# Performance work log

Hardware: AMD Instinct MI355X
Metric: run time of the kernel (lower is better)

The kernel has to match this reference:

```python
import jax, jax.numpy as jnp
import numpy as np

E = 512
H = 8
D = E // H  # 64
B = 2
S = 4096


def setup_inputs() -> dict:
    key = jax.random.key(0)
    ks = jax.random.split(key, 12)
    s = 1.0 / np.sqrt(E)
    return {
        "x": jax.random.normal(ks[0], (B, S, E), dtype=jnp.float32),
        "bias": jax.random.normal(ks[1], (H, 1, S, S), dtype=jnp.float32),
        "mask": jax.random.randint(ks[2], (1, 1, S, S), 0, 2, dtype=jnp.int32),
        "Wq": jax.random.normal(ks[3], (E, E), dtype=jnp.float32) * s,
        "bq": jnp.zeros((E,), dtype=jnp.float32),
        "Wk": jax.random.normal(ks[4], (E, E), dtype=jnp.float32) * s,
        "bk": jnp.zeros((E,), dtype=jnp.float32),
        "Wv": jax.random.normal(ks[5], (E, E), dtype=jnp.float32) * s,
        "bv": jnp.zeros((E,), dtype=jnp.float32),
        "Wo": jax.random.normal(ks[6], (E, E), dtype=jnp.float32) * s,
        "bo": jnp.zeros((E,), dtype=jnp.float32),
    }


def _split_heads(t):
    # [B,S,E] -> [H,B,S,D]  (matches x.view(B,-1,H,D).permute(2,0,1,3))
    b, s, _ = t.shape
    return t.reshape(b, s, H, D).transpose(2, 0, 1, 3)


def reference(x, bias, mask, Wq, bq, Wk, bk, Wv, bv, Wo, bo):
    # torch Linear: y = x @ W.T + b
    q = _split_heads(x @ Wq.T + bq)  # [H,B,S,D]
    k = _split_heads(x @ Wk.T + bk)
    v = _split_heads(x @ Wv.T + bv)

    scores = jnp.einsum("hbqd,hbkd->hbqk", q, k) + bias  # [H,B,S,S]
    scores = jnp.where(mask == 0, jnp.float32(-1e20), scores)
    # NOTE: original divides AFTER bias-add and masking
    probs = jax.nn.softmax(scores / jnp.sqrt(jnp.float32(D)), axis=-1)
    out = jnp.einsum("hbqk,hbkd->hbqd", probs, v)  # [H,B,S,D]
    out = out.transpose(1, 2, 0, 3).reshape(x.shape[0], -1, H * D)  # [B,S,E]
    return out @ Wo.T + bo
```

## Files before the change

### kernel.cpp

```cpp
#include <hip/hip_runtime.h>
#include <hip/hip_bf16.h>

typedef __bf16 bf16x8 __attribute__((ext_vector_type(8)));
typedef float f32x4 __attribute__((ext_vector_type(4)));

#define S_LEN 4096
#define EMB   512
#define NHEAD 8
#define HDIM  64
#define NBAT  2
#define NROW  (NBAT * S_LEN)

static __device__ __forceinline__ f32x4 mfma16x16(bf16x8 a, bf16x8 b, f32x4 c) {
    return __builtin_amdgcn_mfma_f32_16x16x32_bf16(a, b, c, 0, 0, 0);
}

__global__ __launch_bounds__(256) void convert_kernel(
    const float* __restrict__ x, const float* __restrict__ Wq,
    const float* __restrict__ Wk, const float* __restrict__ Wv,
    const float* __restrict__ Wo,
    __hip_bfloat16* __restrict__ xb, __hip_bfloat16* __restrict__ wqkv,
    __hip_bfloat16* __restrict__ wob)
{
    const int NX = NROW * EMB;
    const int NW = EMB * EMB;
    int i = blockIdx.x * 256 + threadIdx.x;
    if (i < NX) { xb[i] = __float2bfloat16(x[i]); return; }
    int j = i - NX;
    if (j < 3 * NW) {
        int p = j >> 18, r = j & (NW - 1);
        const float* src = (p == 0) ? Wq : (p == 1) ? Wk : Wv;
        wqkv[j] = __float2bfloat16(src[r]);
    } else if (j < 4 * NW) {
        int r = j - 3 * NW;
        wob[r] = __float2bfloat16(Wo[r]);
    }
}

__device__ __forceinline__ void gemm_core(
    const __hip_bfloat16* __restrict__ A, const __hip_bfloat16* __restrict__ Bw,
    int mbase, int nbase,
    __hip_bfloat16* As, __hip_bfloat16* Bs, f32x4 acc[2][4])
{
    const int tid = threadIdx.x;
    const int w = tid >> 6, lane = tid & 63, l = lane & 15, quad = lane >> 4;
    const f32x4 zero = {0.f, 0.f, 0.f, 0.f};
#pragma unroll
    for (int mb = 0; mb < 2; mb++)
#pragma unroll
        for (int nb = 0; nb < 4; nb++) acc[mb][nb] = zero;

    const int r0 = tid >> 2, kc = tid & 3;
    const __hip_bfloat16* pa0 = A + (size_t)(mbase + r0) * EMB + kc * 8;
    const __hip_bfloat16* pa1 = pa0 + (size_t)64 * EMB;
    const __hip_bfloat16* pb  = Bw + (size_t)(nbase + r0) * EMB + kc * 8;

    uint4 va0 = *(const uint4*)pa0;
    uint4 va1 = *(const uint4*)pa1;
    uint4 vb  = *(const uint4*)pb;

    for (int k0 = 0; k0 < EMB; k0 += 32) {
        __syncthreads();
        *(uint4*)(As + r0 * 40 + kc * 8)        = va0;
        *(uint4*)(As + (r0 + 64) * 40 + kc * 8) = va1;
        *(uint4*)(Bs + r0 * 40 + kc * 8)        = vb;
        __syncthreads();
        if (k0 + 32 < EMB) {
            va0 = *(const uint4*)(pa0 + k0 + 32);
            va1 = *(const uint4*)(pa1 + k0 + 32);
            vb  = *(const uint4*)(pb  + k0 + 32);
        }
        bf16x8 af[2], bfr[4];
#pragma unroll
        for (int mb = 0; mb < 2; mb++)
            af[mb] = *(const bf16x8*)(As + (w * 32 + mb * 16 + l) * 40 + quad * 8);
#pragma unroll
        for (int nb = 0; nb < 4; nb++)
            bfr[nb] = *(const bf16x8*)(Bs + (nb * 16 + l) * 40 + quad * 8);
        __builtin_amdgcn_s_setprio(1);
#pragma unroll
        for (int mb = 0; mb < 2; mb++)
#pragma unroll
            for (int nb = 0; nb < 4; nb++)
                acc[mb][nb] = mfma16x16(af[mb], bfr[nb], acc[mb][nb]);
        __builtin_amdgcn_s_setprio(0);
    }
}

__global__ __launch_bounds__(256, 4) void qkv_gemm(
    const __hip_bfloat16* __restrict__ xb, const __hip_bfloat16* __restrict__ wqkv,
    const float* __restrict__ bq, const float* __restrict__ bk, const float* __restrict__ bv,
    __hip_bfloat16* __restrict__ Qh, __hip_bfloat16* __restrict__ Kh,
    __hip_bfloat16* __restrict__ Vt)
{
    __shared__ __align__(16) __hip_bfloat16 As[128 * 40];
    __shared__ __align__(16) __hip_bfloat16 Bs[64 * 40];
    const int mbase = blockIdx.x * 128, nbase = blockIdx.y * 64;
    f32x4 acc[2][4];
    gemm_core(xb, wqkv, mbase, nbase, As, Bs, acc);

    const int tid = threadIdx.x;
    const int w = tid >> 6, lane = tid & 63, l = lane & 15, quad = lane >> 4;
    const int p = nbase >> 9;
    const float* bias = (p == 0) ? bq : (p == 1) ? bk : bv;
    __hip_bfloat16* dst = (p == 0) ? Qh : (p == 1) ? Kh : Vt;
#pragma unroll
    for (int mb = 0; mb < 2; mb++)
#pragma unroll
        for (int nb = 0; nb < 4; nb++)
#pragma unroll
            for (int r = 0; r < 4; r++) {
                int m = mbase + w * 32 + mb * 16 + quad * 4 + r;
                int n = nbase + nb * 16 + l;
                int o = n & 511;
                float v = acc[mb][nb][r] + bias[o];
                int b = m >> 12, s = m & 4095, hh = o >> 6, d = o & 63;
                size_t idx = (p == 2)
                    ? ((size_t)((hh * 2 + b) * 64 + d)) * 4096 + s
                    : ((size_t)((hh * 2 + b) * 4096 + s)) * 64 + d;
                dst[idx] = __float2bfloat16(v);
            }
}

__global__ __launch_bounds__(256, 2) void attn_kernel(
    const __hip_bfloat16* __restrict__ Qh, const __hip_bfloat16* __restrict__ Kh,
    const __hip_bfloat16* __restrict__ Vt,
    const float* __restrict__ bias, const int* __restrict__ mask,
    __hip_bfloat16* __restrict__ Om)
{
    const int h = blockIdx.x, qt = blockIdx.y;
    const int tid = threadIdx.x;
    const int w = tid >> 6, lane = tid & 63, l = lane & 15, quad = lane >> 4;
    const int q0 = qt * 64;
    const float CS = 0.18033688011112042f;

    __shared__ __align__(16) __hip_bfloat16 Ks[2][64 * 72];
    __shared__ __align__(16) __hip_bfloat16 Vs[2][64 * 72];
    __shared__ __align__(16) __hip_bfloat16 Ps[64 * 72];
    __shared__ __align__(16) float Bor[64 * 68];

    bf16x8 qf[2][2];
#pragma unroll
    for (int b = 0; b < 2; b++) {
        const __hip_bfloat16* qp =
            Qh + ((size_t)((h * 2 + b) * 4096 + q0 + w * 16 + l)) * 64;
        qf[b][0] = *(const bf16x8*)(qp + quad * 8);
        qf[b][1] = *(const bf16x8*)(qp + 32 + quad * 8);
    }

    f32x4 oacc[2][4];
    float mst[2][4], lst[2][4];
    const f32x4 zero = {0.f, 0.f, 0.f, 0.f};
#pragma unroll
    for (int b = 0; b < 2; b++) {
#pragma unroll
        for (int nb = 0; nb < 4; nb++) oacc[b][nb] = zero;
#pragma unroll
        for (int r = 0; r < 4; r++) { mst[b][r] = -__builtin_inff(); lst[b][r] = 0.f; }
    }

    const int krow = tid >> 3, kch = tid & 7;
    const int ldso0 = krow * 72 + kch * 8;
    const int ldso1 = ldso0 + 32 * 72;
    int koff[8];
#pragma unroll
    for (int j = 0; j < 8; j++) {
        int b = (j >> 1) & 1, isV = j >> 2;
        int row = (j & 1) * 32 + krow;
        koff[j] = isV
            ? ((h * 2 + b) * 64 + row) * 4096 + kch * 8
            : ((h * 2 + b) * 4096 + row) * 64 + kch * 8;
    }
    const float* biasH = bias + (size_t)h * S_LEN * S_LEN;
    int bmo[4], bro[4];
#pragma unroll
    for (int j = 0; j < 4; j++) {
        int d = j * 256 + tid, row = d >> 4, c4 = d & 15;
        bmo[j] = (q0 + row) * S_LEN + c4 * 4;
        bro[j] = row * 68 + c4 * 4;
    }

    uint4  kv[8];
    float4 bv4[4];
    int4   mv4[4];
#pragma unroll
    for (int j = 0; j < 8; j++)
        kv[j] = (j >> 2) ? *(const uint4*)(Vt + koff[j])
                         : *(const uint4*)(Kh + koff[j]);
#pragma unroll
    for (int j = 0; j < 4; j++) {
        bv4[j] = *(const float4*)(biasH + bmo[j]);
        mv4[j] = *(const int4*)(mask + bmo[j]);
    }

    for (int kt = 0; kt < 64; kt++) {
        __syncthreads();
#pragma unroll
        for (int j = 0; j < 8; j++) {
            int lo = (j & 1) ? ldso1 : ldso0;
            if (j >> 2) *(uint4*)(Vs[(j >> 1) & 1] + lo) = kv[j];
            else        *(uint4*)(Ks[(j >> 1) & 1] + lo) = kv[j];
        }
#pragma unroll
        for (int j = 0; j < 4; j++) {
            float4 t;
            t.x = mv4[j].x ? bv4[j].x * CS : -1e30f;
            t.y = mv4[j].y ? bv4[j].y * CS : -1e30f;
            t.z = mv4[j].z ? bv4[j].z * CS : -1e30f;
            t.w = mv4[j].w ? bv4[j].w * CS : -1e30f;
            *(float4*)(Bor + bro[j]) = t;
        }
        __syncthreads();

        if (kt < 63) {
            const int k0 = (kt + 1) * 64;
#pragma unroll
            for (int j = 0; j < 8; j++)
                kv[j] = (j >> 2) ? *(const uint4*)(Vt + koff[j] + k0)
                                 : *(const uint4*)(Kh + koff[j] + k0 * 64);
#pragma unroll
            for (int j = 0; j < 4; j++) {
                bv4[j] = *(const float4*)(biasH + bmo[j] + k0);
                mv4[j] = *(const int4*)(mask + bmo[j] + k0);
            }
        }

        float borr[4][4];
#pragma unroll
        for (int nb = 0; nb < 4; nb++)
#pragma unroll
            for (int r = 0; r < 4; r++)
                borr[nb][r] = Bor[(w * 16 + quad * 4 + r) * 68 + nb * 16 + l];

#pragma unroll
        for (int b = 0; b < 2; b++) {
            f32x4 sc[4] = {zero, zero, zero, zero};
            __builtin_amdgcn_s_setprio(1);
#pragma unroll
            for (int ks = 0; ks < 2; ks++)
#pragma unroll
                for (int nb = 0; nb < 4; nb++) {
                    bf16x8 kf = *(const bf16x8*)(Ks[b] + (nb * 16 + l) * 72 + ks * 32 + quad * 8);
                    sc[nb] = mfma16x16(qf[b][ks], kf, sc[nb]);
                }
            __builtin_amdgcn_s_setprio(0);
            float xv[4][4], rmax[4];
#pragma unroll
            for (int r = 0; r < 4; r++) rmax[r] = -__builtin_inff();
#pragma unroll
            for (int nb = 0; nb < 4; nb++)
#pragma unroll
                for (int r = 0; r < 4; r++) {
                    xv[nb][r] = fmaf(sc[nb][r], CS, borr[nb][r]);
                    rmax[r] = fmaxf(rmax[r], xv[nb][r]);
                }
#pragma unroll
            for (int r = 0; r < 4; r++) {
                rmax[r] = fmaxf(rmax[r], __shfl_xor(rmax[r], 1));
                rmax[r] = fmaxf(rmax[r], __shfl_xor(rmax[r], 2));
                rmax[r] = fmaxf(rmax[r], __shfl_xor(rmax[r], 4));
                rmax[r] = fmaxf(rmax[r], __shfl_xor(rmax[r], 8));
            }
            float alpha[4], rsum[4];
#pragma unroll
            for (int r = 0; r < 4; r++) {
                float mn = fmaxf(mst[b][r], rmax[r]);
                alpha[r] = __builtin_amdgcn_exp2f(mst[b][r] - mn);
                mst[b][r] = mn;
                rsum[r] = 0.f;
            }
#pragma unroll
            for (int nb = 0; nb < 4; nb++)
#pragma unroll
                for (int r = 0; r < 4; r++) {
                    float e = __builtin_amdgcn_exp2f(xv[nb][r] - mst[b][r]);
                    rsum[r] += e;
                    Ps[(w * 16 + quad * 4 + r) * 72 + nb * 16 + l] =
                        __float2bfloat16(e);
                }
#pragma unroll
            for (int r = 0; r < 4; r++) {
                rsum[r] += __shfl_xor(rsum[r], 1);
                rsum[r] += __shfl_xor(rsum[r], 2);
                rsum[r] += __shfl_xor(rsum[r], 4);
                rsum[r] += __shfl_xor(rsum[r], 8);
                lst[b][r] = lst[b][r] * alpha[r] + rsum[r];
            }
#pragma unroll
            for (int nb = 0; nb < 4; nb++)
#pragma unroll
                for (int r = 0; r < 4; r++) oacc[b][nb][r] *= alpha[r];
            __builtin_amdgcn_s_setprio(1);
#pragma unroll
            for (int ks = 0; ks < 2; ks++) {
                bf16x8 pf = *(const bf16x8*)(Ps + (w * 16 + l) * 72 + ks * 32 + quad * 8);
#pragma unroll
                for (int nb = 0; nb < 4; nb++) {
                    bf16x8 vf = *(const bf16x8*)(Vs[b] + (nb * 16 + l) * 72 + ks * 32 + quad * 8);
                    oacc[b][nb] = mfma16x16(pf, vf, oacc[b][nb]);
                }
            }
            __builtin_amdgcn_s_setprio(0);
        }
    }

#pragma unroll
    for (int b = 0; b < 2; b++)
#pragma unroll
        for (int nb = 0; nb < 4; nb++)
#pragma unroll
            for (int r = 0; r < 4; r++) {
                int qq = q0 + w * 16 + quad * 4 + r;
                float val = oacc[b][nb][r] / lst[b][r];
                Om[((size_t)(b * 4096 + qq)) * 512 + h * 64 + nb * 16 + l] =
                    __float2bfloat16(val);
            }
}

__global__ __launch_bounds__(256, 4) void out_gemm(
    const __hip_bfloat16* __restrict__ Om, const __hip_bfloat16* __restrict__ wob,
    const float* __restrict__ bo, float* __restrict__ out)
{
    __shared__ __align__(16) __hip_bfloat16 As[128 * 40];
    __shared__ __align__(16) __hip_bfloat16 Bs[64 * 40];
    const int mbase = blockIdx.x * 128, nbase = blockIdx.y * 64;
    f32x4 acc[2][4];
    gemm_core(Om, wob, mbase, nbase, As, Bs, acc);

    const int tid = threadIdx.x;
    const int w = tid >> 6, lane = tid & 63, l = lane & 15, quad = lane >> 4;
#pragma unroll
    for (int mb = 0; mb < 2; mb++)
#pragma unroll
        for (int nb = 0; nb < 4; nb++)
#pragma unroll
            for (int r = 0; r < 4; r++) {
                int m = mbase + w * 32 + mb * 16 + quad * 4 + r;
                int n = nbase + nb * 16 + l;
                out[(size_t)m * EMB + n] = acc[mb][nb][r] + bo[n];
            }
}

extern "C" void kernel_launch(void* const* d_in, const int* in_sizes, int n_in,
                              void* d_out, int out_size, void* d_ws, size_t ws_size,
                              hipStream_t stream) {
    const float* x    = (const float*)d_in[0];
    const float* bias = (const float*)d_in[1];
    const int*   mask = (const int*)d_in[2];
    const float* Wq   = (const float*)d_in[3];
    const float* bq   = (const float*)d_in[4];
    const float* Wk   = (const float*)d_in[5];
    const float* bk   = (const float*)d_in[6];
    const float* Wv   = (const float*)d_in[7];
    const float* bv   = (const float*)d_in[8];
    const float* Wo   = (const float*)d_in[9];
    const float* bo   = (const float*)d_in[10];
    float* out = (float*)d_out;

    char* ws = (char*)d_ws;
    __hip_bfloat16* xb   = (__hip_bfloat16*)ws; ws += (size_t)NROW * EMB * 2;
    __hip_bfloat16* wqkv = (__hip_bfloat16*)ws; ws += (size_t)3 * EMB * EMB * 2;
    __hip_bfloat16* wob  = (__hip_bfloat16*)ws; ws += (size_t)EMB * EMB * 2;
    __hip_bfloat16* Qh   = (__hip_bfloat16*)ws; ws += (size_t)NROW * EMB * 2;
    __hip_bfloat16* Kh   = (__hip_bfloat16*)ws; ws += (size_t)NROW * EMB * 2;
    __hip_bfloat16* Vt   = (__hip_bfloat16*)ws; ws += (size_t)NROW * EMB * 2;
    __hip_bfloat16* Om   = (__hip_bfloat16*)ws; ws += (size_t)NROW * EMB * 2;

    convert_kernel<<<dim3(20480), dim3(256), 0, stream>>>(
        x, Wq, Wk, Wv, Wo, xb, wqkv, wob);
    qkv_gemm<<<dim3(64, 24), dim3(256), 0, stream>>>(
        xb, wqkv, bq, bk, bv, Qh, Kh, Vt);
    attn_kernel<<<dim3(NHEAD, 64), dim3(256), 0, stream>>>(
        Qh, Kh, Vt, bias, mask, Om);
    out_gemm<<<dim3(64, 8), dim3(256), 0, stream>>>(Om, wob, bo, out);
}
```

Measured before the change: 1.179 ms.

## Pre-tile fp16 bias-mask buffer and stream K/V/bias to LDS asynchronously

Adds a prep kernel that folds the mask and softmax scale into the bias and writes it as a tiled, swizzled fp16 buffer. The attention kernel then loads K, V and bias tiles straight into LDS with global_load_lds, double-buffered, instead of staging them through registers, and splits the two batches' softmax to overlap K prefetch. The V transpose in the QKV GEMM epilogue now goes through LDS for coalesced stores. The cost is an extra full pass over bias and mask plus a large workspace buffer. The original path is kept as a fallback when the workspace is too small.

```diff
diff --git a/kernel.cpp b/kernel.cpp
--- a/kernel.cpp
+++ b/kernel.cpp
@@ -3,6 +3,7 @@
 
 typedef __bf16 bf16x8 __attribute__((ext_vector_type(8)));
 typedef float f32x4 __attribute__((ext_vector_type(4)));
+typedef _Float16 f16x4 __attribute__((ext_vector_type(4)));
 
 #define S_LEN 4096
 #define EMB   512
@@ -13,6 +14,12 @@
 
 static __device__ __forceinline__ f32x4 mfma16x16(bf16x8 a, bf16x8 b, f32x4 c) {
     return __builtin_amdgcn_mfma_f32_16x16x32_bf16(a, b, c, 0, 0, 0);
+}
+
+typedef __attribute__((address_space(1))) const void gas_void;
+typedef __attribute__((address_space(3))) void las_void;
+static __device__ __forceinline__ void gl16(const void* g, void* l) {
+    __builtin_amdgcn_global_load_lds((gas_void*)g, (las_void*)l, 16, 0, 0);
 }
 
 __global__ __launch_bounds__(256) void convert_kernel(
@@ -37,6 +44,30 @@
     }
 }
 
+__global__ __launch_bounds__(256) void prep_kernel(
+    const float* __restrict__ bias, const int* __restrict__ mask,
+    _Float16* __restrict__ Bm)
+{
+    const float CS = 0.18033688011112042f;
+    int i = blockIdx.x * 256 + threadIdx.x;
+    int h = i >> 22;
+    int rem = i & ((1 << 22) - 1);
+    int q = rem >> 10;
+    int k = (rem & 1023) << 2;
+    float4 b4 = *(const float4*)(bias + ((size_t)h * S_LEN + q) * S_LEN + k);
+    int4   m4 = *(const int4*)(mask + (size_t)q * S_LEN + k);
+    int row = q & 63, kcol = k & 63;
+    int colp = (kcol & 15) | ((((kcol >> 4) ^ ((row >> 2) & 3)) & 3) << 4);
+    size_t dst = ((size_t)((h * 64 + (q >> 6)) * 64 + (k >> 6))) * 4096
+               + row * 64 + colp;
+    f16x4 o;
+    o[0] = (_Float16)(m4.x ? b4.x * CS : -60000.f);
+    o[1] = (_Float16)(m4.y ? b4.y * CS : -60000.f);
+    o[2] = (_Float16)(m4.z ? b4.z * CS : -60000.f);
+    o[3] = (_Float16)(m4.w ? b4.w * CS : -60000.f);
+    *(f16x4*)(Bm + dst) = o;
+}
+
 __device__ __forceinline__ void gemm_core(
     const __hip_bfloat16* __restrict__ A, const __hip_bfloat16* __restrict__ Bw,
     int mbase, int nbase,
@@ -95,6 +126,7 @@
 {
     __shared__ __align__(16) __hip_bfloat16 As[128 * 40];
     __shared__ __align__(16) __hip_bfloat16 Bs[64 * 40];
+    __shared__ __align__(16) __hip_bfloat16 Ts[64 * 136];
     const int mbase = blockIdx.x * 128, nbase = blockIdx.y * 64;
     f32x4 acc[2][4];
     gemm_core(xb, wqkv, mbase, nbase, As, Bs, acc);
@@ -103,7 +135,31 @@
     const int w = tid >> 6, lane = tid & 63, l = lane & 15, quad = lane >> 4;
     const int p = nbase >> 9;
     const float* bias = (p == 0) ? bq : (p == 1) ? bk : bv;
-    __hip_bfloat16* dst = (p == 0) ? Qh : (p == 1) ? Kh : Vt;
+
+    if (p == 2) {
+#pragma unroll
+        for (int mb = 0; mb < 2; mb++)
+#pragma unroll
+            for (int nb = 0; nb < 4; nb++)
+#pragma unroll
+                for (int r = 0; r < 4; r++) {
+                    int sl = w * 32 + mb * 16 + quad * 4 + r;
+                    int d  = nb * 16 + l;
+                    float v = acc[mb][nb][r] + bias[(nbase & 511) + d];
+                    Ts[d * 136 + sl] = __float2bfloat16(v);
+                }
+        __syncthreads();
+        const int b = mbase >> 12, s0 = mbase & 4095;
+        const int hh = (nbase & 511) >> 6;
+#pragma unroll
+        for (int c = tid; c < 1024; c += 256) {
+            int d = c >> 4, sc = c & 15;
+            uint4 v = *(const uint4*)(Ts + d * 136 + sc * 8);
+            *(uint4*)(Vt + ((size_t)((hh * 2 + b) * 64 + d)) * 4096 + s0 + sc * 8) = v;
+        }
+        return;
+    }
+    __hip_bfloat16* dst = (p == 0) ? Qh : Kh;
 #pragma unroll
     for (int mb = 0; mb < 2; mb++)
 #pragma unroll
@@ -115,14 +171,271 @@
                 int o = n & 511;
                 float v = acc[mb][nb][r] + bias[o];
                 int b = m >> 12, s = m & 4095, hh = o >> 6, d = o & 63;
-                size_t idx = (p == 2)
-                    ? ((size_t)((hh * 2 + b) * 64 + d)) * 4096 + s
-                    : ((size_t)((hh * 2 + b) * 4096 + s)) * 64 + d;
-                dst[idx] = __float2bfloat16(v);
+                dst[((size_t)((hh * 2 + b) * 4096 + s)) * 64 + d] = __float2bfloat16(v);
             }
 }
 
 __global__ __launch_bounds__(256, 2) void attn_kernel(
+    const __hip_bfloat16* __restrict__ Qh, const __hip_bfloat16* __restrict__ Kh,
+    const __hip_bfloat16* __restrict__ Vt, const _Float16* __restrict__ Bm,
+    __hip_bfloat16* __restrict__ Om)
+{
+    const int h = blockIdx.x, qt = blockIdx.y;
+    const int tid = threadIdx.x;
+    const int w = tid >> 6, lane = tid & 63, l = lane & 15, quad = lane >> 4;
+    const int q0 = qt * 64;
+    const float CS = 0.18033688011112042f;
+
+    __shared__ __align__(16) __hip_bfloat16 Kl[2][4096];
+    __shared__ __align__(16) __hip_bfloat16 Vl[2][2][4096];
+    __shared__ __align__(16) _Float16      BmL[2][4096];
+    __shared__ __align__(16) __hip_bfloat16 Ps[64 * 72];
+
+    const int swz  = ((lane & 7) ^ ((lane >> 3) & 7)) << 3;
+    const int kpat = ((lane >> 3) << 6) + swz;
+    const int vpat = ((lane >> 3) << 12) + swz;
+
+    const int wb = w & 1, wi4 = (w >> 1) * 4;
+    const __hip_bfloat16* Kbase = Kh + ((size_t)((h * 2 + wb) * 4096)) * 64;
+    const __hip_bfloat16* Vbase = Vt + ((size_t)((h * 2 + wb) * 64)) * 4096;
+    const _Float16*       Bbase = Bm + ((size_t)((h * 64 + qt) * 64)) * 4096;
+
+    bf16x8 qf[2][2];
+#pragma unroll
+    for (int b = 0; b < 2; b++) {
+        const __hip_bfloat16* qp =
+            Qh + ((size_t)((h * 2 + b) * 4096 + q0 + w * 16 + l)) * 64;
+        qf[b][0] = *(const bf16x8*)(qp + quad * 8);
+        qf[b][1] = *(const bf16x8*)(qp + 32 + quad * 8);
+    }
+
+    f32x4 oacc[2][4];
+    float mst[2][4], lst[2][4];
+    const f32x4 zero = {0.f, 0.f, 0.f, 0.f};
+#pragma unroll
+    for (int b = 0; b < 2; b++) {
+#pragma unroll
+        for (int nb = 0; nb < 4; nb++) oacc[b][nb] = zero;
+#pragma unroll
+        for (int r = 0; r < 4; r++) { mst[b][r] = -__builtin_inff(); lst[b][r] = 0.f; }
+    }
+
+    {
+        const __hip_bfloat16* kb = Kbase;
+#pragma unroll
+        for (int j = 0; j < 4; j++) {
+            int i = wi4 + j;
+            gl16(kb + i * 512 + kpat, Kl[wb] + i * 512);
+        }
+        const __hip_bfloat16* vb = Vbase;
+#pragma unroll
+        for (int j = 0; j < 4; j++) {
+            int i = wi4 + j;
+            gl16(vb + (size_t)i * 32768 + vpat, Vl[0][wb] + i * 512);
+        }
+        const _Float16* bb = Bbase;
+#pragma unroll
+        for (int j = 0; j < 2; j++) {
+            int i = w * 2 + j;
+            gl16(bb + i * 512 + lane * 8, BmL[0] + i * 512);
+        }
+    }
+
+    for (int kt = 0; kt < 64; kt++) {
+        const int cur = kt & 1, nxt = cur ^ 1;
+        __syncthreads();
+
+        if (kt < 63) {
+            const __hip_bfloat16* vb = Vbase + (kt + 1) * 64;
+#pragma unroll
+            for (int j = 0; j < 4; j++) {
+                int i = wi4 + j;
+                gl16(vb + (size_t)i * 32768 + vpat, Vl[nxt][wb] + i * 512);
+            }
+            const _Float16* bb = Bbase + (size_t)(kt + 1) * 4096;
+#pragma unroll
+            for (int j = 0; j < 2; j++) {
+                int i = w * 2 + j;
+                gl16(bb + i * 512 + lane * 8, BmL[nxt] + i * 512);
+            }
+        }
+
+        float borr[4][4];
+#pragma unroll
+        for (int nb = 0; nb < 4; nb++)
+#pragma unroll
+            for (int r = 0; r < 4; r++) {
+                int row = w * 16 + quad * 4 + r;
+                borr[nb][r] =
+                    (float)BmL[cur][row * 64 + (((nb ^ quad) & 3) << 4) + l];
+            }
+
+        f32x4 sc1[4] = {zero, zero, zero, zero};
+#pragma unroll
+        for (int b = 0; b < 2; b++) {
+            f32x4 sc[4] = {zero, zero, zero, zero};
+            __builtin_amdgcn_s_setprio(1);
+#pragma unroll
+            for (int ks = 0; ks < 2; ks++)
+#pragma unroll
+                for (int nb = 0; nb < 4; nb++) {
+                    bf16x8 kf = *(const bf16x8*)(
+                        Kl[b] + ((nb * 16 + l) << 6) + (((ks * 4 + quad) ^ (l & 7)) << 3));
+                    sc[nb] = mfma16x16(qf[b][ks], kf, sc[nb]);
+                }
+            __builtin_amdgcn_s_setprio(0);
+
+            if (b == 1) {
+#pragma unroll
+                for (int nb = 0; nb < 4; nb++) sc1[nb] = sc[nb];
+                break;
+            }
+            float xv[4][4], rmax[4];
+#pragma unroll
+            for (int r = 0; r < 4; r++) rmax[r] = -__builtin_inff();
+#pragma unroll
+            for (int nb = 0; nb < 4; nb++)
+#pragma unroll
+                for (int r = 0; r < 4; r++) {
+                    xv[nb][r] = fmaf(sc[nb][r], CS, borr[nb][r]);
+                    rmax[r] = fmaxf(rmax[r], xv[nb][r]);
+                }
+#pragma unroll
+            for (int r = 0; r < 4; r++) {
+                rmax[r] = fmaxf(rmax[r], __shfl_xor(rmax[r], 1));
+                rmax[r] = fmaxf(rmax[r], __shfl_xor(rmax[r], 2));
+                rmax[r] = fmaxf(rmax[r], __shfl_xor(rmax[r], 4));
+                rmax[r] = fmaxf(rmax[r], __shfl_xor(rmax[r], 8));
+            }
+            float alpha[4], rsum[4];
+#pragma unroll
+            for (int r = 0; r < 4; r++) {
+                float mn = fmaxf(mst[0][r], rmax[r]);
+                alpha[r] = __builtin_amdgcn_exp2f(mst[0][r] - mn);
+                mst[0][r] = mn;
+                rsum[r] = 0.f;
+            }
+#pragma unroll
+            for (int nb = 0; nb < 4; nb++)
+#pragma unroll
+                for (int r = 0; r < 4; r++) {
+                    float e = __builtin_amdgcn_exp2f(xv[nb][r] - mst[0][r]);
+                    rsum[r] += e;
+                    Ps[(w * 16 + quad * 4 + r) * 72 + nb * 16 + l] =
+                        __float2bfloat16(e);
+                }
+#pragma unroll
+            for (int r = 0; r < 4; r++) {
+                rsum[r] += __shfl_xor(rsum[r], 1);
+                rsum[r] += __shfl_xor(rsum[r], 2);
+                rsum[r] += __shfl_xor(rsum[r], 4);
+                rsum[r] += __shfl_xor(rsum[r], 8);
+                lst[0][r] = lst[0][r] * alpha[r] + rsum[r];
+            }
+#pragma unroll
+            for (int nb = 0; nb < 4; nb++)
+#pragma unroll
+                for (int r = 0; r < 4; r++) oacc[0][nb][r] *= alpha[r];
+            __builtin_amdgcn_s_setprio(1);
+#pragma unroll
+            for (int ks = 0; ks < 2; ks++) {
+                bf16x8 pf = *(const bf16x8*)(Ps + (w * 16 + l) * 72 + ks * 32 + quad * 8);
+#pragma unroll
+                for (int nb = 0; nb < 4; nb++) {
+                    bf16x8 vf = *(const bf16x8*)(
+                        Vl[cur][0] + ((nb * 16 + l) << 6) + (((ks * 4 + quad) ^ (l & 7)) << 3));
+                    oacc[0][nb] = mfma16x16(pf, vf, oacc[0][nb]);
+                }
+            }
+            __builtin_amdgcn_s_setprio(0);
+        }
+
+        __syncthreads();
+        if (kt < 63) {
+            const __hip_bfloat16* kb = Kbase + (size_t)(kt + 1) * 64 * 64;
+#pragma unroll
+            for (int j = 0; j < 4; j++) {
+                int i = wi4 + j;
+                gl16(kb + i * 512 + kpat, Kl[wb] + i * 512);
+            }
+        }
+
+        {
+            float xv[4][4], rmax[4];
+#pragma unroll
+            for (int r = 0; r < 4; r++) rmax[r] = -__builtin_inff();
+#pragma unroll
+            for (int nb = 0; nb < 4; nb++)
+#pragma unroll
+                for (int r = 0; r < 4; r++) {
+                    xv[nb][r] = fmaf(sc1[nb][r], CS, borr[nb][r]);
+                    rmax[r] = fmaxf(rmax[r], xv[nb][r]);
+                }
+#pragma unroll
+            for (int r = 0; r < 4; r++) {
+                rmax[r] = fmaxf(rmax[r], __shfl_xor(rmax[r], 1));
+                rmax[r] = fmaxf(rmax[r], __shfl_xor(rmax[r], 2));
+                rmax[r] = fmaxf(rmax[r], __shfl_xor(rmax[r], 4));
+                rmax[r] = fmaxf(rmax[r], __shfl_xor(rmax[r], 8));
+            }
+            float alpha[4], rsum[4];
+#pragma unroll
+            for (int r = 0; r < 4; r++) {
+                float mn = fmaxf(mst[1][r], rmax[r]);
+                alpha[r] = __builtin_amdgcn_exp2f(mst[1][r] - mn);
+                mst[1][r] = mn;
+                rsum[r] = 0.f;
+            }
+#pragma unroll
+            for (int nb = 0; nb < 4; nb++)
+#pragma unroll
+                for (int r = 0; r < 4; r++) {
+                    float e = __builtin_amdgcn_exp2f(xv[nb][r] - mst[1][r]);
+                    rsum[r] += e;
+                    Ps[(w * 16 + quad * 4 + r) * 72 + nb * 16 + l] =
+                        __float2bfloat16(e);
+                }
+#pragma unroll
+            for (int r = 0; r < 4; r++) {
+                rsum[r] += __shfl_xor(rsum[r], 1);
+                rsum[r] += __shfl_xor(rsum[r], 2);
+                rsum[r] += __shfl_xor(rsum[r], 4);
+                rsum[r] += __shfl_xor(rsum[r], 8);
+                lst[1][r] = lst[1][r] * alpha[r] + rsum[r];
+            }
+#pragma unroll
+            for (int nb = 0; nb < 4; nb++)
+#pragma unroll
+                for (int r = 0; r < 4; r++) oacc[1][nb][r] *= alpha[r];
+            __builtin_amdgcn_s_setprio(1);
+#pragma unroll
+            for (int ks = 0; ks < 2; ks++) {
+                bf16x8 pf = *(const bf16x8*)(Ps + (w * 16 + l) * 72 + ks * 32 + quad * 8);
+#pragma unroll
+                for (int nb = 0; nb < 4; nb++) {
+                    bf16x8 vf = *(const bf16x8*)(
+                        Vl[cur][1] + ((nb * 16 + l) << 6) + (((ks * 4 + quad) ^ (l & 7)) << 3));
+                    oacc[1][nb] = mfma16x16(pf, vf, oacc[1][nb]);
+                }
+            }
+            __builtin_amdgcn_s_setprio(0);
+        }
+    }
+
+#pragma unroll
+    for (int b = 0; b < 2; b++)
+#pragma unroll
+        for (int nb = 0; nb < 4; nb++)
+#pragma unroll
+            for (int r = 0; r < 4; r++) {
+                int qq = q0 + w * 16 + quad * 4 + r;
+                float val = oacc[b][nb][r] / lst[b][r];
+                Om[((size_t)(b * 4096 + qq)) * 512 + h * 64 + nb * 16 + l] =
+                    __float2bfloat16(val);
+            }
+}
+
+__global__ __launch_bounds__(256, 2) void attn_fallback(
     const __hip_bfloat16* __restrict__ Qh, const __hip_bfloat16* __restrict__ Kh,
     const __hip_bfloat16* __restrict__ Vt,
     const float* __restrict__ bias, const int* __restrict__ mask,
@@ -147,7 +460,6 @@
         qf[b][0] = *(const bf16x8*)(qp + quad * 8);
         qf[b][1] = *(const bf16x8*)(qp + 32 + quad * 8);
     }
-
     f32x4 oacc[2][4];
     float mst[2][4], lst[2][4];
     const f32x4 zero = {0.f, 0.f, 0.f, 0.f};
@@ -158,7 +470,6 @@
 #pragma unroll
         for (int r = 0; r < 4; r++) { mst[b][r] = -__builtin_inff(); lst[b][r] = 0.f; }
     }
-
     const int krow = tid >> 3, kch = tid & 7;
     const int ldso0 = krow * 72 + kch * 8;
     const int ldso1 = ldso0 + 32 * 72;
@@ -179,20 +490,15 @@
         bmo[j] = (q0 + row) * S_LEN + c4 * 4;
         bro[j] = row * 68 + c4 * 4;
     }
-
-    uint4  kv[8];
-    float4 bv4[4];
-    int4   mv4[4];
+    uint4 kv[8]; float4 bv4[4]; int4 mv4[4];
 #pragma unroll
     for (int j = 0; j < 8; j++)
-        kv[j] = (j >> 2) ? *(const uint4*)(Vt + koff[j])
-                         : *(const uint4*)(Kh + koff[j]);
+        kv[j] = (j >> 2) ? *(const uint4*)(Vt + koff[j]) : *(const uint4*)(Kh + koff[j]);
 #pragma unroll
     for (int j = 0; j < 4; j++) {
         bv4[j] = *(const float4*)(biasH + bmo[j]);
         mv4[j] = *(const int4*)(mask + bmo[j]);
     }
-
     for (int kt = 0; kt < 64; kt++) {
         __syncthreads();
 #pragma unroll
@@ -211,7 +517,6 @@
             *(float4*)(Bor + bro[j]) = t;
         }
         __syncthreads();
-
         if (kt < 63) {
             const int k0 = (kt + 1) * 64;
 #pragma unroll
@@ -224,14 +529,12 @@
                 mv4[j] = *(const int4*)(mask + bmo[j] + k0);
             }
         }
-
         float borr[4][4];
 #pragma unroll
         for (int nb = 0; nb < 4; nb++)
 #pragma unroll
             for (int r = 0; r < 4; r++)
                 borr[nb][r] = Bor[(w * 16 + quad * 4 + r) * 68 + nb * 16 + l];
-
 #pragma unroll
         for (int b = 0; b < 2; b++) {
             f32x4 sc[4] = {zero, zero, zero, zero};
@@ -275,8 +578,7 @@
                 for (int r = 0; r < 4; r++) {
                     float e = __builtin_amdgcn_exp2f(xv[nb][r] - mst[b][r]);
                     rsum[r] += e;
-                    Ps[(w * 16 + quad * 4 + r) * 72 + nb * 16 + l] =
-                        __float2bfloat16(e);
+                    Ps[(w * 16 + quad * 4 + r) * 72 + nb * 16 + l] = __float2bfloat16(e);
                 }
 #pragma unroll
             for (int r = 0; r < 4; r++) {
@@ -303,7 +605,6 @@
             __builtin_amdgcn_s_setprio(0);
         }
     }
-
 #pragma unroll
     for (int b = 0; b < 2; b++)
 #pragma unroll
@@ -358,19 +659,29 @@
     float* out = (float*)d_out;
 
     char* ws = (char*)d_ws;
-    __hip_bfloat16* xb   = (__hip_bfloat16*)ws; ws += (size_t)NROW * EMB * 2;
-    __hip_bfloat16* wqkv = (__hip_bfloat16*)ws; ws += (size_t)3 * EMB * EMB * 2;
-    __hip_bfloat16* wob  = (__hip_bfloat16*)ws; ws += (size_t)EMB * EMB * 2;
-    __hip_bfloat16* Qh   = (__hip_bfloat16*)ws; ws += (size_t)NROW * EMB * 2;
-    __hip_bfloat16* Kh   = (__hip_bfloat16*)ws; ws += (size_t)NROW * EMB * 2;
-    __hip_bfloat16* Vt   = (__hip_bfloat16*)ws; ws += (size_t)NROW * EMB * 2;
-    __hip_bfloat16* Om   = (__hip_bfloat16*)ws; ws += (size_t)NROW * EMB * 2;
+    size_t off = 0;
+    __hip_bfloat16* xb   = (__hip_bfloat16*)(ws + off); off += (size_t)NROW * EMB * 2;
+    __hip_bfloat16* wqkv = (__hip_bfloat16*)(ws + off); off += (size_t)3 * EMB * EMB * 2;
+    __hip_bfloat16* wob  = (__hip_bfloat16*)(ws + off); off += (size_t)EMB * EMB * 2;
+    __hip_bfloat16* Qh   = (__hip_bfloat16*)(ws + off); off += (size_t)NROW * EMB * 2;
+    __hip_bfloat16* Kh   = (__hip_bfloat16*)(ws + off); off += (size_t)NROW * EMB * 2;
+    __hip_bfloat16* Vt   = (__hip_bfloat16*)(ws + off); off += (size_t)NROW * EMB * 2;
+    __hip_bfloat16* Om   = (__hip_bfloat16*)(ws + off); off += (size_t)NROW * EMB * 2;
+    _Float16*       Bm   = (_Float16*)(ws + off);
+    const size_t BMBYTES = (size_t)NHEAD * S_LEN * S_LEN * 2;
+    const bool bmok = ws_size >= off + BMBYTES;
 
     convert_kernel<<<dim3(20480), dim3(256), 0, stream>>>(
         x, Wq, Wk, Wv, Wo, xb, wqkv, wob);
     qkv_gemm<<<dim3(64, 24), dim3(256), 0, stream>>>(
         xb, wqkv, bq, bk, bv, Qh, Kh, Vt);
-    attn_kernel<<<dim3(NHEAD, 64), dim3(256), 0, stream>>>(
-        Qh, Kh, Vt, bias, mask, Om);
+    if (bmok) {
+        prep_kernel<<<dim3(131072), dim3(256), 0, stream>>>(bias, mask, Bm);
+        attn_kernel<<<dim3(NHEAD, 64), dim3(256), 0, stream>>>(
+            Qh, Kh, Vt, Bm, Om);
+    } else {
+        attn_fallback<<<dim3(NHEAD, 64), dim3(256), 0, stream>>>(
+            Qh, Kh, Vt, bias, mask, Om);
+    }
     out_gemm<<<dim3(64, 8), dim3(256), 0, stream>>>(Om, wob, bo, out);
 }
```

After: 1.112 ms. 1.06x faster.
